# Optimization experiments

Hardware: AMD Instinct MI355X
Metric: run time of the kernel (lower is better)

The kernel has to match this reference:

```python
import jax, jax.numpy as jnp
import numpy as np

NUM_HEADS = 16
LN_EPS = 1e-12


def setup_inputs() -> dict:
    key = jax.random.key(0)
    ks = jax.random.split(key, 4)
    L, B, D = 2048, 2, 1024
    x = jax.random.normal(ks[0], (L, B, D), dtype=jnp.float32)
    attention_mask = jax.random.randint(ks[1], (B, L), 0, 2, dtype=jnp.int32)
    ln_w = jnp.ones((D,), dtype=jnp.float32)
    ln_b = jnp.zeros((D,), dtype=jnp.float32)
    qkv_w = jax.random.normal(ks[2], (3 * D, D), dtype=jnp.float32) * 0.02
    qkv_b = jnp.zeros((3 * D,), dtype=jnp.float32)
    out_w = jax.random.normal(ks[3], (D, D), dtype=jnp.float32) * 0.02
    out_b = jnp.zeros((D,), dtype=jnp.float32)
    return {"x": x, "attention_mask": attention_mask, "ln_w": ln_w, "ln_b": ln_b,
            "qkv_w": qkv_w, "qkv_b": qkv_b, "out_w": out_w, "out_b": out_b}


def _layer_norm(x, w, b):
    mu = jnp.mean(x, axis=-1, keepdims=True)
    var = jnp.mean(jnp.square(x - mu), axis=-1, keepdims=True)
    return (x - mu) * jax.lax.rsqrt(var + LN_EPS) * w + b


def reference(x, attention_mask, ln_w, ln_b, qkv_w, qkv_b, out_w, out_b):
    L, B, D = x.shape
    H = NUM_HEADS
    hd = D // H
    scale = 1.0 / np.sqrt(hd).astype(np.float32)

    xn = _layer_norm(x, ln_w, ln_b)                       # (L, B, D)
    qkv = xn @ qkv_w.T + qkv_b                            # (L, B, 3D)
    q, k, v = jnp.split(qkv, 3, axis=-1)
    # (L, B, D) -> (L, B*H, hd) -> (B*H, L, hd)
    q = q.reshape(L, B * H, hd).swapaxes(0, 1)
    k = k.reshape(L, B * H, hd).swapaxes(0, 1)
    v = v.reshape(L, B * H, hd).swapaxes(0, 1)

    scores = jnp.einsum('nld,nmd->nlm', q, k) * scale     # (B*H, L, L)
    mask = jnp.broadcast_to(attention_mask[:, None, :], (B, H, L)).reshape(B * H, 1, L)
    scores = jnp.where(mask == 0, -jnp.inf, scores)
    probs = jax.nn.softmax(scores, axis=-1)               # masked cols -> 0
    # dropout prob = 0.0 -> identity
    context = jnp.einsum('nlm,nmd->nld', probs, v)        # (B*H, L, hd)
    context = context.swapaxes(0, 1).reshape(L, B, D)
    return context @ out_w.T + out_b
```

## Files before the change

kernel.cpp:

```cpp
#include <hip/hip_runtime.h>
#include <hip/hip_bf16.h>
#include <cstdint>

static constexpr int LSEQ = 2048;
static constexpr int BB   = 2;
static constexpr int DM   = 1024;
static constexpr int NHD  = 16;
static constexpr int HD   = 64;
static constexpr int ROWS = LSEQ * BB;
static constexpr int NQKV = 3 * DM;

typedef __attribute__((ext_vector_type(8)))  short v8s;
typedef __attribute__((ext_vector_type(4)))  float v4f;
typedef __attribute__((ext_vector_type(16))) float v16f;
typedef __attribute__((ext_vector_type(4)))  unsigned int v4u;

#if __has_builtin(__builtin_amdgcn_exp2f)
#define EXP2F(x) __builtin_amdgcn_exp2f(x)
#else
#define EXP2F(x) __expf((x) * 0.69314718056f)
#endif

static constexpr float QSCALE = 0.125f * 1.44269504089f;
static constexpr float NEGM   = -10.0f * 1.44269504089f;

__device__ __forceinline__ unsigned short f2bf(float f) {
    unsigned int u = __builtin_bit_cast(unsigned int, f);
    u += 0x7fffu + ((u >> 16) & 1u);
    return (unsigned short)(u >> 16);
}

__device__ __forceinline__ void gload_lds16(const void* g, void* l) {
    auto gp = (const __attribute__((address_space(1))) unsigned int*)(uintptr_t)g;
    auto lp = (__attribute__((address_space(3))) unsigned int*)(uintptr_t)l;
    __builtin_amdgcn_global_load_lds(gp, lp, 16, 0, 0);
}

__global__ __launch_bounds__(256) void cast_w_kernel(const float* __restrict__ qkv_w,
                                                     const float* __restrict__ out_w,
                                                     unsigned short* __restrict__ wq,
                                                     unsigned short* __restrict__ wo) {
    size_t i = ((size_t)blockIdx.x * 256 + threadIdx.x) * 8;
    const float* src; unsigned short* dst; size_t off;
    if (i < (size_t)NQKV * DM) { src = qkv_w; dst = wq; off = i; }
    else                       { src = out_w; dst = wo; off = i - (size_t)NQKV * DM; }
    float4 a = *(const float4*)(src + off);
    float4 b = *(const float4*)(src + off + 4);
    ushort4 o0, o1;
    o0.x = f2bf(a.x); o0.y = f2bf(a.y); o0.z = f2bf(a.z); o0.w = f2bf(a.w);
    o1.x = f2bf(b.x); o1.y = f2bf(b.y); o1.z = f2bf(b.z); o1.w = f2bf(b.w);
    *(ushort4*)(dst + off)     = o0;
    *(ushort4*)(dst + off + 4) = o1;
}

__global__ __launch_bounds__(256) void ln_cast_kernel(const float* __restrict__ x,
                                                      const float* __restrict__ w,
                                                      const float* __restrict__ bia,
                                                      unsigned short* __restrict__ xn) {
    const int row = blockIdx.x;
    const int t = threadIdx.x;
    const float* xr = x + (size_t)row * DM;
    float4 v = ((const float4*)xr)[t];
    float s  = v.x + v.y + v.z + v.w;
    float sq = v.x*v.x + v.y*v.y + v.z*v.z + v.w*v.w;
    #pragma unroll
    for (int off = 32; off > 0; off >>= 1) {
        s  += __shfl_down(s, off);
        sq += __shfl_down(sq, off);
    }
    __shared__ float red[8];
    const int wv = t >> 6;
    if ((t & 63) == 0) { red[wv] = s; red[4 + wv] = sq; }
    __syncthreads();
    if (t == 0) {
        float S = red[0] + red[1] + red[2] + red[3];
        float Q = red[4] + red[5] + red[6] + red[7];
        float mu  = S * (1.0f / DM);
        float var = Q * (1.0f / DM) - mu * mu;
        red[0] = mu;
        red[1] = rsqrtf(var + 1e-12f);
    }
    __syncthreads();
    const float mu = red[0], rs = red[1];
    float4 wv4 = ((const float4*)w)[t];
    float4 bv4 = ((const float4*)bia)[t];
    ushort4 o;
    o.x = f2bf((v.x - mu) * rs * wv4.x + bv4.x);
    o.y = f2bf((v.y - mu) * rs * wv4.y + bv4.y);
    o.z = f2bf((v.z - mu) * rs * wv4.z + bv4.z);
    o.w = f2bf((v.w - mu) * rs * wv4.w + bv4.w);
    ((ushort4*)(xn + (size_t)row * DM))[t] = o;
}

template <int BM, int BN, int EPI>
__global__ __launch_bounds__(BM == 256 ? 512 : 256)
void gemm2_kernel(const unsigned short* __restrict__ A,
                  const unsigned short* __restrict__ Bt,
                  const float* __restrict__ bias,
                  float* __restrict__ outF,
                  unsigned short* __restrict__ qb,
                  unsigned short* __restrict__ kb,
                  unsigned short* __restrict__ vt,
                  int N) {
    constexpr int K  = DM;
    constexpr int NW = (BM == 256) ? 8 : 4;
    constexpr int NWN = NW / 2;
    constexpr int WM = BM / 2;
    constexpr int WN = BN / NWN;
    constexpr int MR = WM / 16;
    constexpr int FC = WN / 16;
    constexpr int NT = K / 64;
    constexpr int LPS = (BM + BN) / NW / 8;
    __shared__ unsigned short Al[2][BM * 64];
    __shared__ unsigned short Bl[2][BN * 64];
    const int nbn = N / BN;
    const int cpx = gridDim.x >> 3;
    const int sid = (blockIdx.x & 7) * cpx + (blockIdx.x >> 3);
    const int bm = sid / nbn;
    const int bn = sid % nbn;
    const int tid = threadIdx.x;
    const int w = tid >> 6, lane = tid & 63;
    const int l15 = lane & 15, l4 = lane >> 4;
    const int wm = w / NWN, wn = w % NWN;
    const unsigned short* Ab = A  + (size_t)bm * BM * K;
    const unsigned short* Bb = Bt + (size_t)bn * BN * K;
    const int srow8  = lane >> 3;
    const int schunk = ((lane & 7) ^ (srow8 & 7)) * 8;
    const int swz    = l15 & 7;

    v4f acc[MR][FC] = {};

    auto STAGE = [&](int buf, int t) {
        const int k0 = t * 64;
        #pragma unroll
        for (int i = 0; i < BM / 8 / NW; ++i) {
            const int r0 = w * (BM / NW) + i * 8;
            gload_lds16(Ab + (size_t)(r0 + srow8) * K + k0 + schunk, &Al[buf][r0 * 64]);
        }
        #pragma unroll
        for (int i = 0; i < BN / 8 / NW; ++i) {
            const int r0 = w * (BN / NW) + i * 8;
            gload_lds16(Bb + (size_t)(r0 + srow8) * K + k0 + schunk, &Bl[buf][r0 * 64]);
        }
    };
    auto COMPUTE = [&](int buf) {
        #pragma unroll
        for (int ks = 0; ks < 2; ++ks) {
            v8s af[MR]; v8s bf[FC];
            #pragma unroll
            for (int m = 0; m < MR; ++m) {
                const int row = wm * WM + m * 16 + l15;
                af[m] = *(const v8s*)&Al[buf][row * 64 + ((ks * 4 + l4) ^ swz) * 8];
            }
            #pragma unroll
            for (int n = 0; n < FC; ++n) {
                const int row = wn * WN + n * 16 + l15;
                bf[n] = *(const v8s*)&Bl[buf][row * 64 + ((ks * 4 + l4) ^ swz) * 8];
            }
            #pragma unroll
            for (int m = 0; m < MR; ++m)
                #pragma unroll
                for (int n = 0; n < FC; ++n)
                    acc[m][n] = __builtin_amdgcn_mfma_f32_16x16x32_bf16(af[m], bf[n], acc[m][n], 0, 0, 0);
        }
    };

    STAGE(0, 0);
    int cur = 0;
    for (int t = 0; t < NT; ++t) {
        if (t + 1 < NT) {
            STAGE(cur ^ 1, t + 1);
            if constexpr (LPS == 7)      asm volatile("s_waitcnt vmcnt(7)" ::: "memory");
            else if constexpr (LPS == 6) asm volatile("s_waitcnt vmcnt(6)" ::: "memory");
            else if constexpr (LPS == 5) asm volatile("s_waitcnt vmcnt(5)" ::: "memory");
            else                         asm volatile("s_waitcnt vmcnt(0)" ::: "memory");
        } else {
            asm volatile("s_waitcnt vmcnt(0)" ::: "memory");
        }
        __builtin_amdgcn_s_barrier();
        __builtin_amdgcn_sched_barrier(0);
        COMPUTE(cur);
        __builtin_amdgcn_s_barrier();
        cur ^= 1;
    }

    #pragma unroll
    for (int m = 0; m < MR; ++m) {
        #pragma unroll
        for (int n = 0; n < FC; ++n) {
            #pragma unroll
            for (int r = 0; r < 4; ++r) {
                const int row = bm * BM + wm * WM + m * 16 + l4 * 4 + r;
                const int col = bn * BN + wn * WN + n * 16 + l15;
                const float val = acc[m][n][r] + bias[col];
                if (EPI == 0) {
                    outF[(size_t)row * N + col] = val;
                } else {
                    const int lq = row >> 1, b = row & 1;
                    const int which = col >> 10, jr = col & 1023;
                    const int h = jr >> 6, d = jr & 63;
                    const int bh = b * NHD + h;
                    if (which == 0)      qb[((size_t)bh * LSEQ + lq) * HD + d] = f2bf(val * QSCALE);
                    else if (which == 1) kb[((size_t)bh * LSEQ + lq) * HD + d] = f2bf(val);
                    else                 vt[((size_t)bh * HD + d) * LSEQ + lq] = f2bf(val);
                }
            }
        }
    }
}

__global__ __launch_bounds__(256) void attn_kernel(const unsigned short* __restrict__ qbuf,
                                                   const unsigned short* __restrict__ kbuf,
                                                   const unsigned short* __restrict__ vtbuf,
                                                   const int* __restrict__ amask,
                                                   unsigned short* __restrict__ ctx) {
    __shared__ unsigned short Kl[2][64 * 64];
    __shared__ unsigned short Vl[2][64 * 64];
    __shared__ alignas(16) float mb_all[LSEQ];
    __shared__ alignas(16) float inv_l[4 * 32];
    const int id = blockIdx.x;
    const int inner = id >> 3;
    const int bh = (id & 7) * 4 + (inner & 3);
    const int qblk = inner >> 2;
    const int bat = bh >> 4, h = bh & 15;
    const int tid = threadIdx.x;
    const int w = tid >> 6, lane = tid & 63;
    const int l31 = lane & 31, hi = lane >> 5;
    const int q0 = qblk * 128 + w * 32;

    #pragma unroll
    for (int i = 0; i < LSEQ / 256; ++i)
        mb_all[i * 256 + tid] = amask[bat * LSEQ + i * 256 + tid] ? NEGM : -1e30f;

    const unsigned short* Qp = qbuf + ((size_t)bh * LSEQ + q0 + l31) * HD + hi * 8;
    v8s qfr[4];
    #pragma unroll
    for (int s = 0; s < 4; ++s) qfr[s] = *(const v8s*)(Qp + s * 16);

    const unsigned short* Kb = kbuf  + (size_t)bh * LSEQ * HD;
    const unsigned short* Vb = vtbuf + (size_t)bh * HD * LSEQ;

    v16f O0 = {}, O1 = {};
    float lsum = 0.f;

    const int srow = lane >> 3;
    const int schunk = ((lane & 7) ^ srow) * 8;
    const int rsw = l31 & 7;

    auto STAGE = [&](int buf, int kv0) {
        const int r0 = w * 16;
        gload_lds16(Kb + (size_t)(kv0 + r0 + srow) * HD + schunk,       &Kl[buf][r0 * 64]);
        gload_lds16(Kb + (size_t)(kv0 + r0 + 8 + srow) * HD + schunk,   &Kl[buf][(r0 + 8) * 64]);
        gload_lds16(Vb + (size_t)(r0 + srow) * LSEQ + kv0 + schunk,     &Vl[buf][r0 * 64]);
        gload_lds16(Vb + (size_t)(r0 + 8 + srow) * LSEQ + kv0 + schunk, &Vl[buf][(r0 + 8) * 64]);
    };

    STAGE(0, 0);
    __syncthreads();
    int cur = 0;
    for (int t = 0; t < LSEQ / 64; ++t) {
        if (t + 1 < LSEQ / 64) STAGE(cur ^ 1, (t + 1) * 64);
        const int kv0 = t * 64;

        #pragma unroll
        for (int kvh = 0; kvh < 2; ++kvh) {
            v16f sc = {};
            #pragma unroll
            for (int s = 0; s < 4; ++s) {
                const v8s kf = *(const v8s*)&Kl[cur][(kvh * 32 + l31) * 64 + ((2 * s + hi) ^ rsw) * 8];
                sc = __builtin_amdgcn_mfma_f32_32x32x16_bf16(kf, qfr[s], sc, 0, 0, 0);
            }
            float4 mbv[4];
            #pragma unroll
            for (int g = 0; g < 4; ++g)
                mbv[g] = *(const float4*)&mb_all[kv0 + kvh * 32 + g * 8 + hi * 4];
            float pf[16];
            #pragma unroll
            for (int g = 0; g < 4; ++g) {
                #pragma unroll
                for (int bq = 0; bq < 4; ++bq) {
                    const float mbx = (bq == 0) ? mbv[g].x : (bq == 1) ? mbv[g].y
                                     : (bq == 2) ? mbv[g].z : mbv[g].w;
                    const float p = EXP2F(sc[g * 4 + bq] + mbx);
                    pf[g * 4 + bq] = p;
                    lsum += p;
                }
            }
            #pragma unroll
            for (int c = 0; c < 2; ++c) {
                unsigned int W[4];
                #pragma unroll
                for (int k = 0; k < 4; ++k)
                    asm("v_cvt_pk_bf16_f32 %0, %1, %2"
                        : "=v"(W[k]) : "v"(pf[8 * c + 2 * k]), "v"(pf[8 * c + 2 * k + 1]));
                const unsigned int sel0 = hi ? W[0] : W[2];
                const unsigned int sel1 = hi ? W[1] : W[3];
                const unsigned int S0 = (unsigned int)__shfl_xor((int)sel0, 32);
                const unsigned int S1 = (unsigned int)__shfl_xor((int)sel1, 32);
                v4u fw;
                fw.x = hi ? S0 : W[0];
                fw.y = hi ? S1 : W[1];
                fw.z = hi ? W[2] : S0;
                fw.w = hi ? W[3] : S1;
                const v8s pa = __builtin_bit_cast(v8s, fw);
                const int vch = (kvh * 4 + c * 2 + hi);
                const v8s vf0 = *(const v8s*)&Vl[cur][(l31) * 64      + (vch ^ rsw) * 8];
                const v8s vf1 = *(const v8s*)&Vl[cur][(32 + l31) * 64 + (vch ^ rsw) * 8];
                O0 = __builtin_amdgcn_mfma_f32_32x32x16_bf16(pa, vf0, O0, 0, 0, 0);
                O1 = __builtin_amdgcn_mfma_f32_32x32x16_bf16(pa, vf1, O1, 0, 0, 0);
            }
        }
        __syncthreads();
        cur ^= 1;
    }

    lsum += __shfl_xor(lsum, 32);
    if (hi == 0) inv_l[w * 32 + l31] = 1.0f / lsum;
    asm volatile("s_waitcnt lgkmcnt(0)" ::: "memory");
    __builtin_amdgcn_sched_barrier(0);

    #pragma unroll
    for (int g = 0; g < 4; ++g) {
        const float4 iv = *(const float4*)&inv_l[w * 32 + g * 8 + hi * 4];
        #pragma unroll
        for (int bq = 0; bq < 4; ++bq) {
            const float ivx = (bq == 0) ? iv.x : (bq == 1) ? iv.y : (bq == 2) ? iv.z : iv.w;
            const int lq = q0 + g * 8 + hi * 4 + bq;
            unsigned short* crow = ctx + ((size_t)lq * BB + bat) * DM + h * HD;
            crow[l31]      = f2bf(O0[g * 4 + bq] * ivx);
            crow[32 + l31] = f2bf(O1[g * 4 + bq] * ivx);
        }
    }
}

extern "C" void kernel_launch(void* const* d_in, const int* in_sizes, int n_in,
                              void* d_out, int out_size, void* d_ws, size_t ws_size,
                              hipStream_t stream) {
    (void)in_sizes; (void)n_in; (void)out_size; (void)ws_size;
    const float* x     = (const float*)d_in[0];
    const int*   amask = (const int*)d_in[1];
    const float* ln_w  = (const float*)d_in[2];
    const float* ln_b  = (const float*)d_in[3];
    const float* qkv_w = (const float*)d_in[4];
    const float* qkv_b = (const float*)d_in[5];
    const float* out_w = (const float*)d_in[6];
    const float* out_b = (const float*)d_in[7];
    float* out = (float*)d_out;

    unsigned short* ws    = (unsigned short*)d_ws;
    unsigned short* xn    = ws;
    unsigned short* wq    = xn + (size_t)ROWS * DM;
    unsigned short* wo    = wq + (size_t)NQKV * DM;
    unsigned short* qbuf  = wo + (size_t)DM * DM;
    unsigned short* kbuf  = qbuf + (size_t)BB * NHD * LSEQ * HD;
    unsigned short* vtbuf = kbuf + (size_t)BB * NHD * LSEQ * HD;
    unsigned short* ctx   = vtbuf + (size_t)BB * NHD * LSEQ * HD;

    cast_w_kernel<<<2048, 256, 0, stream>>>(qkv_w, out_w, wq, wo);
    ln_cast_kernel<<<ROWS, 256, 0, stream>>>(x, ln_w, ln_b, xn);
    gemm2_kernel<256, 192, 1><<<(ROWS / 256) * (NQKV / 192), 512, 0, stream>>>(
        xn, wq, qkv_b, nullptr, qbuf, kbuf, vtbuf, NQKV);
    attn_kernel<<<512, 256, 0, stream>>>(qbuf, kbuf, vtbuf, amask, ctx);
    gemm2_kernel<128, 64, 0><<<(ROWS / 128) * (DM / 64), 256, 0, stream>>>(
        ctx, wo, out_b, out, nullptr, nullptr, nullptr, DM);
}
```

Measured before the change: 127.9 us.

## Add ping-pong scheduled QKV GEMM kernel with split staging and priority

Replaces the templated 256x192 QKV GEMM with a dedicated kernel that splits each K-tile into four LDS-read/MFMA phases. Global-to-LDS staging for the next tile is interleaved between the phases in three pieces (A halves and B), and MFMA clusters run at raised wave priority via s_setprio. The aim is to overlap memory traffic with matrix math and cut stalls at the single barrier per tile. The cost is many more barriers per iteration and tighter vmcnt accounting that could serialize waves.

After: 128.2 us. Within noise of the previous version (+0.3%).

```diff
diff --git a/kernel.cpp b/kernel.cpp
--- a/kernel.cpp
+++ b/kernel.cpp
@@ -92,18 +92,145 @@
     ((ushort4*)(xn + (size_t)row * DM))[t] = o;
 }
 
-template <int BM, int BN, int EPI>
-__global__ __launch_bounds__(BM == 256 ? 512 : 256)
+__global__ __launch_bounds__(512) void gemm8p_kernel(const unsigned short* __restrict__ A,
+                                                     const unsigned short* __restrict__ Bt,
+                                                     const float* __restrict__ bias,
+                                                     unsigned short* __restrict__ qb,
+                                                     unsigned short* __restrict__ kb,
+                                                     unsigned short* __restrict__ vt) {
+    constexpr int K  = DM;
+    constexpr int NT = K / 64;
+    __shared__ unsigned short Al[2][256 * 64];
+    __shared__ unsigned short Bl[2][192 * 64];
+    constexpr int nbn = NQKV / 192;
+    const int cpx = gridDim.x >> 3;
+    const int sid = (blockIdx.x & 7) * cpx + (blockIdx.x >> 3);
+    const int bm = sid / nbn;
+    const int bn = sid % nbn;
+    const int tid = threadIdx.x;
+    const int w = tid >> 6, lane = tid & 63;
+    const int l15 = lane & 15, l4 = lane >> 4;
+    const int wm = w >> 2, wn = w & 3;
+    const unsigned short* Ab = A  + (size_t)bm * 256 * K;
+    const unsigned short* Bb = Bt + (size_t)bn * 192 * K;
+    const int srow8  = lane >> 3;
+    const int schunk = ((lane & 7) ^ (srow8 & 7)) * 8;
+    const int swz    = l15 & 7;
+
+    v4f acc[8][3] = {};
+    v8s af[4], bf[3];
+
+    auto stageA0 = [&](int buf, int t) {
+        const int k0 = t * 64;
+        #pragma unroll
+        for (int i = 0; i < 2; ++i) {
+            const int r0 = w * 16 + i * 8;
+            gload_lds16(Ab + (size_t)(r0 + srow8) * K + k0 + schunk, &Al[buf][r0 * 64]);
+        }
+    };
+    auto stageA1 = [&](int buf, int t) {
+        const int k0 = t * 64;
+        #pragma unroll
+        for (int i = 0; i < 2; ++i) {
+            const int r0 = 128 + w * 16 + i * 8;
+            gload_lds16(Ab + (size_t)(r0 + srow8) * K + k0 + schunk, &Al[buf][r0 * 64]);
+        }
+    };
+    auto stageB = [&](int buf, int t) {
+        const int k0 = t * 64;
+        #pragma unroll
+        for (int i = 0; i < 3; ++i) {
+            const int r0 = w * 24 + i * 8;
+            gload_lds16(Bb + (size_t)(r0 + srow8) * K + k0 + schunk, &Bl[buf][r0 * 64]);
+        }
+    };
+    auto DSREAD = [&](int buf, int mh, int ks) {
+        #pragma unroll
+        for (int m = 0; m < 4; ++m) {
+            const int row = wm * 128 + (mh * 4 + m) * 16 + l15;
+            af[m] = *(const v8s*)&Al[buf][row * 64 + ((ks * 4 + l4) ^ swz) * 8];
+        }
+        #pragma unroll
+        for (int n = 0; n < 3; ++n) {
+            const int row = wn * 48 + n * 16 + l15;
+            bf[n] = *(const v8s*)&Bl[buf][row * 64 + ((ks * 4 + l4) ^ swz) * 8];
+        }
+    };
+    auto MFMACL = [&](int mh) {
+        __builtin_amdgcn_s_setprio(1);
+        #pragma unroll
+        for (int m = 0; m < 4; ++m)
+            #pragma unroll
+            for (int n = 0; n < 3; ++n)
+                acc[mh * 4 + m][n] =
+                    __builtin_amdgcn_mfma_f32_16x16x32_bf16(af[m], bf[n], acc[mh * 4 + m][n], 0, 0, 0);
+        __builtin_amdgcn_s_setprio(0);
+    };
+#define LGKM0 do { asm volatile("s_waitcnt lgkmcnt(0)" ::: "memory"); \
+                   __builtin_amdgcn_sched_barrier(0); } while (0)
+
+    stageA0(0, 0); stageA1(0, 0); stageB(0, 0);
+    int cur = 0;
+    for (int t = 0; t < NT; ++t) {
+        const bool last = (t == NT - 1);
+        if (!last) {
+            stageA0(cur ^ 1, t + 1);
+            asm volatile("s_waitcnt vmcnt(2)" ::: "memory");
+        } else {
+            asm volatile("s_waitcnt vmcnt(0)" ::: "memory");
+        }
+        __builtin_amdgcn_s_barrier();
+        __builtin_amdgcn_sched_barrier(0);
+        DSREAD(cur, 0, 0); LGKM0; MFMACL(0);
+        __builtin_amdgcn_s_barrier();
+        DSREAD(cur, 1, 0);
+        if (!last) stageA1(cur ^ 1, t + 1);
+        __builtin_amdgcn_s_barrier();
+        LGKM0; MFMACL(1);
+        __builtin_amdgcn_s_barrier();
+        DSREAD(cur, 0, 1);
+        if (!last) stageB(cur ^ 1, t + 1);
+        __builtin_amdgcn_s_barrier();
+        LGKM0; MFMACL(0);
+        __builtin_amdgcn_s_barrier();
+        DSREAD(cur, 1, 1);
+        __builtin_amdgcn_s_barrier();
+        LGKM0; MFMACL(1);
+        __builtin_amdgcn_s_barrier();
+        cur ^= 1;
+    }
+#undef LGKM0
+
+    #pragma unroll
+    for (int m = 0; m < 8; ++m) {
+        #pragma unroll
+        for (int n = 0; n < 3; ++n) {
+            #pragma unroll
+            for (int r = 0; r < 4; ++r) {
+                const int row = bm * 256 + wm * 128 + m * 16 + l4 * 4 + r;
+                const int col = bn * 192 + wn * 48 + n * 16 + l15;
+                const float val = acc[m][n][r] + bias[col];
+                const int lq = row >> 1, b = row & 1;
+                const int which = col >> 10, jr = col & 1023;
+                const int h = jr >> 6, d = jr & 63;
+                const int bh = b * NHD + h;
+                if (which == 0)      qb[((size_t)bh * LSEQ + lq) * HD + d] = f2bf(val * QSCALE);
+                else if (which == 1) kb[((size_t)bh * LSEQ + lq) * HD + d] = f2bf(val);
+                else                 vt[((size_t)bh * HD + d) * LSEQ + lq] = f2bf(val);
+            }
+        }
+    }
+}
+
+template <int BM, int BN>
+__global__ __launch_bounds__(256)
 void gemm2_kernel(const unsigned short* __restrict__ A,
                   const unsigned short* __restrict__ Bt,
                   const float* __restrict__ bias,
                   float* __restrict__ outF,
-                  unsigned short* __restrict__ qb,
-                  unsigned short* __restrict__ kb,
-                  unsigned short* __restrict__ vt,
                   int N) {
     constexpr int K  = DM;
-    constexpr int NW = (BM == 256) ? 8 : 4;
+    constexpr int NW = 4;
     constexpr int NWN = NW / 2;
     constexpr int WM = BM / 2;
     constexpr int WN = BN / NWN;
@@ -170,10 +297,8 @@
     for (int t = 0; t < NT; ++t) {
         if (t + 1 < NT) {
             STAGE(cur ^ 1, t + 1);
-            if constexpr (LPS == 7)      asm volatile("s_waitcnt vmcnt(7)" ::: "memory");
-            else if constexpr (LPS == 6) asm volatile("s_waitcnt vmcnt(6)" ::: "memory");
-            else if constexpr (LPS == 5) asm volatile("s_waitcnt vmcnt(5)" ::: "memory");
-            else                         asm volatile("s_waitcnt vmcnt(0)" ::: "memory");
+            if constexpr (LPS == 6) asm volatile("s_waitcnt vmcnt(6)" ::: "memory");
+            else                    asm volatile("s_waitcnt vmcnt(0)" ::: "memory");
         } else {
             asm volatile("s_waitcnt vmcnt(0)" ::: "memory");
         }
@@ -185,28 +310,15 @@
     }
 
     #pragma unroll
-    for (int m = 0; m < MR; ++m) {
-        #pragma unroll
-        for (int n = 0; n < FC; ++n) {
+    for (int m = 0; m < MR; ++m)
+        #pragma unroll
+        for (int n = 0; n < FC; ++n)
             #pragma unroll
             for (int r = 0; r < 4; ++r) {
                 const int row = bm * BM + wm * WM + m * 16 + l4 * 4 + r;
                 const int col = bn * BN + wn * WN + n * 16 + l15;
-                const float val = acc[m][n][r] + bias[col];
-                if (EPI == 0) {
-                    outF[(size_t)row * N + col] = val;
-                } else {
-                    const int lq = row >> 1, b = row & 1;
-                    const int which = col >> 10, jr = col & 1023;
-                    const int h = jr >> 6, d = jr & 63;
-                    const int bh = b * NHD + h;
-                    if (which == 0)      qb[((size_t)bh * LSEQ + lq) * HD + d] = f2bf(val * QSCALE);
-                    else if (which == 1) kb[((size_t)bh * LSEQ + lq) * HD + d] = f2bf(val);
-                    else                 vt[((size_t)bh * HD + d) * LSEQ + lq] = f2bf(val);
-                }
-            }
-        }
-    }
+                outF[(size_t)row * N + col] = acc[m][n][r] + bias[col];
+            }
 }
 
 __global__ __launch_bounds__(256) void attn_kernel(const unsigned short* __restrict__ qbuf,
@@ -358,9 +470,9 @@
 
     cast_w_kernel<<<2048, 256, 0, stream>>>(qkv_w, out_w, wq, wo);
     ln_cast_kernel<<<ROWS, 256, 0, stream>>>(x, ln_w, ln_b, xn);
-    gemm2_kernel<256, 192, 1><<<(ROWS / 256) * (NQKV / 192), 512, 0, stream>>>(
-        xn, wq, qkv_b, nullptr, qbuf, kbuf, vtbuf, NQKV);
+    gemm8p_kernel<<<(ROWS / 256) * (NQKV / 192), 512, 0, stream>>>(
+        xn, wq, qkv_b, qbuf, kbuf, vtbuf);
     attn_kernel<<<512, 256, 0, stream>>>(qbuf, kbuf, vtbuf, amask, ctx);
-    gemm2_kernel<128, 64, 0><<<(ROWS / 128) * (DM / 64), 256, 0, stream>>>(
-        ctx, wo, out_b, out, nullptr, nullptr, nullptr, DM);
-}
+    gemm2_kernel<128, 64><<<(ROWS / 128) * (DM / 64), 256, 0, stream>>>(
+        ctx, wo, out_b, out, DM);
+}
```
